# Optimization experiments

Hardware: AMD Instinct MI355X
Metric: run time of the kernel (lower is better)

Reference implementation:

```python
import jax, jax.numpy as jnp
import numpy as np

HIDDEN = 1024
HEADS = 16
HEAD_DIM = HIDDEN // HEADS


def setup_inputs() -> dict:
    key = jax.random.key(0)
    k0, k1, k2, k3, k4 = jax.random.split(key, 5)
    s = 0.02
    return {
        "data": jax.random.normal(k0, (4, 2048, HIDDEN), dtype=jnp.float32),
        "qkv_w": jax.random.normal(k1, (3 * HIDDEN, HIDDEN), dtype=jnp.float32) * s,  # (out,in) torch layout
        "qkv_b": jax.random.normal(k2, (3 * HIDDEN,), dtype=jnp.float32) * s,
        "out_w": jax.random.normal(k3, (HIDDEN, HIDDEN), dtype=jnp.float32) * s,
        "out_b": jax.random.normal(k4, (HIDDEN,), dtype=jnp.float32) * s,
    }


def reference(data, qkv_w, qkv_b, out_w, out_b):
    B, T, C = data.shape
    qkv = jnp.einsum("btc,oc->bto", data, qkv_w) + qkv_b  # [B,T,3C]
    q, k, v = jnp.split(qkv, 3, axis=2)
    # [B,T,C] -> [B,H,T,D]
    def heads(x):
        return x.reshape(B, T, HEADS, HEAD_DIM).transpose(0, 2, 1, 3)
    q, k, v = heads(q), heads(k), heads(v)
    scale = 1.0 / jnp.sqrt(jnp.float32(HEAD_DIM))
    att = jnp.einsum("bhqd,bhkd->bhqk", q, k) * scale  # [B,H,T,T]
    causal = jnp.tril(jnp.ones((T, T), dtype=bool))
    att = jnp.where(causal[None, None, :, :], att, -jnp.inf)
    att = jax.nn.softmax(att, axis=-1)
    out = jnp.einsum("bhqk,bhkd->bhqd", att, v)  # [B,H,T,D]
    out = out.transpose(0, 2, 1, 3).reshape(B, T, C)
    return jnp.einsum("btc,oc->bto", out, out_w) + out_b
```

## Files before the change

### kernel.cpp

```cpp
#include <hip/hip_runtime.h>
#include <hip/hip_bf16.h>
#include <stdint.h>

typedef __attribute__((ext_vector_type(8))) __bf16 bf16x8;
typedef __attribute__((ext_vector_type(4))) float f32x4;
typedef __attribute__((ext_vector_type(16))) float f32x16;
typedef __attribute__((ext_vector_type(4))) unsigned int u32x4;

#define HIDDEN 1024
#define HEADS 16
#define HD 64
#define NB 4
#define T_ 2048
#define M_ROWS (NB * T_)
#define SCL2 0.18033688f
#define FIXM 32.0f

__device__ __forceinline__ unsigned short f2bf(float x) {
  unsigned u = __builtin_bit_cast(unsigned, x);
  u += 0x7fff + ((u >> 16) & 1);
  return (unsigned short)(u >> 16);
}

__device__ __forceinline__ unsigned pk2(float a, float b) {
  unsigned ua = __builtin_bit_cast(unsigned, a) + 0x8000u;
  unsigned ub = __builtin_bit_cast(unsigned, b) + 0x8000u;
  return __builtin_amdgcn_perm(ub, ua, 0x07060302);
}

__device__ __forceinline__ f32x4 mfma16(bf16x8 a, bf16x8 b, f32x4 c) {
  return __builtin_amdgcn_mfma_f32_16x16x32_bf16(a, b, c, 0, 0, 0);
}
__device__ __forceinline__ f32x16 mfma32(bf16x8 a, bf16x8 b, f32x16 c) {
  return __builtin_amdgcn_mfma_f32_32x32x16_bf16(a, b, c, 0, 0, 0);
}

__device__ __forceinline__ void lds16(const void* g, void* l) {
  __builtin_amdgcn_global_load_lds(
      (const __attribute__((address_space(1))) unsigned int*)g,
      (__attribute__((address_space(3))) unsigned int*)l, 16, 0, 0);
}

__device__ __forceinline__ bf16x8 ldg8(const unsigned short* p) {
  return __builtin_bit_cast(bf16x8, *(const u32x4*)p);
}

__global__ void cvt_bf16(const float* __restrict__ in,
                         unsigned short* __restrict__ out, int n4) {
  int i = blockIdx.x * blockDim.x + threadIdx.x;
  int stride = gridDim.x * blockDim.x;
  for (; i < n4; i += stride) {
    float4 v = ((const float4*)in)[i];
    ushort4 o;
    o.x = f2bf(v.x); o.y = f2bf(v.y); o.z = f2bf(v.z); o.w = f2bf(v.w);
    ((ushort4*)out)[i] = o;
  }
}

template <int EPI>
__global__ __launch_bounds__(256) void gemm_bt(
    const unsigned short* __restrict__ A, const unsigned short* __restrict__ Bm,
    const float* __restrict__ bias, unsigned short* __restrict__ Qb,
    unsigned short* __restrict__ Kb, unsigned short* __restrict__ Vtb,
    float* __restrict__ Cf, int M, int N, int K) {
  __shared__ __align__(16) unsigned short Al[128 * 32];
  __shared__ __align__(16) unsigned short Bl[128 * 32];
  const int tid = threadIdx.x;
  const int w = tid >> 6, lane = tid & 63;
  const int l16 = lane & 15, grp = lane >> 4;
  const int brow0 = blockIdx.y * 128;
  const int bcol0 = blockIdx.x * 128;
  const int wrow = (w >> 1) * 64, wcol = (w & 1) * 64;

  f32x4 acc[4][4];
#pragma unroll
  for (int i = 0; i < 4; i++)
#pragma unroll
    for (int j = 0; j < 4; j++) acc[i][j] = (f32x4){0.f, 0.f, 0.f, 0.f};

  for (int k0 = 0; k0 < K; k0 += 32) {
    __syncthreads();
#pragma unroll
    for (int i = 0; i < 2; i++) {
      int off = (w * 2 + i) * 1024 + lane * 16;
      int row = off >> 6;
      int cole = (off & 63) >> 1;
      lds16(A + (size_t)(brow0 + row) * K + k0 + cole,
            (char*)Al + (w * 2 + i) * 1024);
      lds16(Bm + (size_t)(bcol0 + row) * K + k0 + cole,
            (char*)Bl + (w * 2 + i) * 1024);
    }
    __syncthreads();
    bf16x8 av[4], bv[4];
#pragma unroll
    for (int m = 0; m < 4; m++)
      av[m] = __builtin_bit_cast(
          bf16x8, *(const u32x4*)&Al[(wrow + m * 16 + l16) * 32 + grp * 8]);
#pragma unroll
    for (int n = 0; n < 4; n++)
      bv[n] = __builtin_bit_cast(
          bf16x8, *(const u32x4*)&Bl[(wcol + n * 16 + l16) * 32 + grp * 8]);
#pragma unroll
    for (int m = 0; m < 4; m++)
#pragma unroll
      for (int n = 0; n < 4; n++) acc[m][n] = mfma16(av[m], bv[n], acc[m][n]);
  }

#pragma unroll
  for (int m = 0; m < 4; m++) {
#pragma unroll
    for (int n = 0; n < 4; n++) {
      int col = bcol0 + wcol + n * 16 + l16;
      int row0 = brow0 + wrow + m * 16 + grp * 4;
      float bs = bias[col];
      if (EPI == 0) {
        int part = col >> 10, rem = col & 1023;
        int h = rem >> 6, d = rem & 63;
#pragma unroll
        for (int r = 0; r < 4; r++) {
          int rw = row0 + r;
          int b = rw >> 11, t = rw & 2047;
          unsigned short val = f2bf(acc[m][n][r] + bs);
          size_t bh = (size_t)(b * 16 + h);
          if (part == 0)
            Qb[(bh * T_ + t) * HD + d] = val;
          else if (part == 1)
            Kb[(bh * T_ + t) * HD + d] = val;
          else {
            int k = t & 31;
            int rr = (k & 3) + 4 * (k >> 3);
            int s = (rr & 7) + 8 * ((k >> 2) & 1) + 16 * (rr >> 3);
            Vtb[(bh * HD + d) * T_ + (t & ~31) + s] = val;
          }
        }
      } else {
#pragma unroll
        for (int r = 0; r < 4; r++)
          Cf[(size_t)(row0 + r) * N + col] = acc[m][n][r] + bs;
      }
    }
  }
}


__global__ __launch_bounds__(256, 3) void attn32(
    const unsigned short* __restrict__ Q, const unsigned short* __restrict__ K,
    const unsigned short* __restrict__ Vt, unsigned short* __restrict__ Ao) {
  __shared__ __align__(16) unsigned short Kl[2][32 * 64];
  __shared__ __align__(16) unsigned short Vl[2][32 * 64];
  const int i = blockIdx.x;
  const int bh = i & 63;
  const int g = (i < 512) ? (15 - (i >> 6)) : ((i - 512) >> 6);
  const int wv = threadIdx.x >> 6, lane = threadIdx.x & 63;
  const int l31 = lane & 31, hi = lane >> 5;
  const int qt = g * 4 + wv;
  const int maxqt = g * 4 + 3;
  const unsigned short* Qh = Q + (size_t)bh * T_ * HD;
  const unsigned short* Kh = K + (size_t)bh * T_ * HD;
  const unsigned short* Vh = Vt + (size_t)bh * HD * T_;
  const int b_ = bh >> 4, h_ = bh & 15;

  const int sj = threadIdx.x >> 3, su = threadIdx.x & 7;
  const int sup = su ^ (sj & 7);
  const unsigned short* ksrc = Kh + sj * HD + sup * 8;
  const unsigned short* vsrc =
      Vh + (size_t)(sj + 32 * (sup >> 2)) * T_ + (sup & 3) * 8;
  char* kdst0 = (char*)&Kl[0][0] + wv * 1024;
  char* kdst1 = (char*)&Kl[1][0] + wv * 1024;
  char* vdst0 = (char*)&Vl[0][0] + wv * 1024;
  char* vdst1 = (char*)&Vl[1][0] + wv * 1024;

#define STAGE(B, KC)                                         \
  do {                                                       \
    int kt_ = (KC) * 32;                                     \
    lds16(ksrc + (size_t)kt_ * HD, (B) ? kdst1 : kdst0);     \
    lds16(vsrc + kt_, (B) ? vdst1 : vdst0);                  \
  } while (0)

  int rdoff[4];
#pragma unroll
  for (int ks = 0; ks < 4; ks++)
    rdoff[ks] = l31 * 128 + (((2 * ks + hi) ^ (l31 & 7)) << 4);

  bf16x8 qf[4];
  const int qbase = qt * 32;
#pragma unroll
  for (int st = 0; st < 4; st++)
    qf[st] = ldg8(&Qh[(size_t)(qbase + l31) * HD + st * 16 + hi * 8]);

  f32x16 o0, o1;
#pragma unroll
  for (int r = 0; r < 16; r++) { o0[r] = 0.f; o1[r] = 0.f; }
  float rl = 0.f;

#define CHUNK(B, MASKED)                                                     \
  do {                                                                       \
    const char* kb = (const char*)&Kl[(B)][0];                               \
    const char* vb = (const char*)&Vl[(B)][0];                               \
    bf16x8 KF[4], VF[4];                                                     \
    _Pragma("unroll") for (int ks = 0; ks < 4; ks++) {                       \
      KF[ks] = __builtin_bit_cast(bf16x8, *(const u32x4*)(kb + rdoff[ks]));  \
      VF[ks] = __builtin_bit_cast(bf16x8, *(const u32x4*)(vb + rdoff[ks]));  \
    }                                                                        \
    f32x16 sa;                                                               \
    _Pragma("unroll") for (int r = 0; r < 16; r++) sa[r] = 0.f;              \
    sa = mfma32(KF[0], qf[0], sa);                                           \
    sa = mfma32(KF[1], qf[1], sa);                                           \
    sa = mfma32(KF[2], qf[2], sa);                                           \
    sa = mfma32(KF[3], qf[3], sa);                                           \
    float pv[16];                                                            \
    _Pragma("unroll") for (int r = 0; r < 16; r++) {                         \
      float arg = __builtin_fmaf(sa[r], SCL2, -FIXM);                        \
      if (MASKED) {                                                          \
        int key = (r & 3) + 8 * (r >> 2) + 4 * hi;                           \
        if (key > l31) arg = -1e30f;                                         \
      }                                                                      \
      pv[r] = exp2f(arg);                                                    \
      rl += pv[r];                                                           \
    }                                                                        \
    u32x4 pa0u, pa1u;                                                        \
    pa0u.x = pk2(pv[0], pv[1]);                                              \
    pa0u.y = pk2(pv[2], pv[3]);                                              \
    pa0u.z = pk2(pv[4], pv[5]);                                              \
    pa0u.w = pk2(pv[6], pv[7]);                                              \
    pa1u.x = pk2(pv[8], pv[9]);                                              \
    pa1u.y = pk2(pv[10], pv[11]);                                            \
    pa1u.z = pk2(pv[12], pv[13]);                                            \
    pa1u.w = pk2(pv[14], pv[15]);                                            \
    bf16x8 pa0 = __builtin_bit_cast(bf16x8, pa0u);                           \
    bf16x8 pa1 = __builtin_bit_cast(bf16x8, pa1u);                           \
    o0 = mfma32(VF[0], pa0, o0);                                             \
    o0 = mfma32(VF[1], pa1, o0);                                             \
    o1 = mfma32(VF[2], pa0, o1);                                             \
    o1 = mfma32(VF[3], pa1, o1);                                             \
  } while (0)

  STAGE(0, 0);
  __syncthreads();
  int cur = 0;
  for (int kc = 0; kc <= maxqt; kc++) {
    if (kc < maxqt) STAGE(cur ^ 1, kc + 1);
    if (kc < qt) {
      CHUNK(cur, 0);
    } else if (kc == qt) {
      CHUNK(cur, 1);
    }
    __syncthreads();
    cur ^= 1;
  }

  float rlt = rl + __shfl_xor(rl, 32);
  float inv = 1.f / rlt;
  const size_t base =
      ((size_t)b_ * T_ + qbase + l31) * HIDDEN + h_ * HD + hi * 4;
#pragma unroll
  for (int gg = 0; gg < 4; gg++) {
    uint2 u;
    u.x = pk2(o0[4 * gg] * inv, o0[4 * gg + 1] * inv);
    u.y = pk2(o0[4 * gg + 2] * inv, o0[4 * gg + 3] * inv);
    *(uint2*)&Ao[base + gg * 8] = u;
  }
#pragma unroll
  for (int gg = 0; gg < 4; gg++) {
    uint2 u;
    u.x = pk2(o1[4 * gg] * inv, o1[4 * gg + 1] * inv);
    u.y = pk2(o1[4 * gg + 2] * inv, o1[4 * gg + 3] * inv);
    *(uint2*)&Ao[base + 32 + gg * 8] = u;
  }
#undef STAGE
#undef CHUNK
}

extern "C" void kernel_launch(void* const* d_in, const int* in_sizes, int n_in,
                              void* d_out, int out_size, void* d_ws,
                              size_t ws_size, hipStream_t stream) {
  const float* data = (const float*)d_in[0];
  const float* qkvw = (const float*)d_in[1];
  const float* qkvb = (const float*)d_in[2];
  const float* outw = (const float*)d_in[3];
  const float* outb = (const float*)d_in[4];
  float* out = (float*)d_out;
  char* ws = (char*)d_ws;

  unsigned short* dataBf = (unsigned short*)(ws);
  unsigned short* qkvwBf = (unsigned short*)(ws + 16777216);
  unsigned short* outwBf = (unsigned short*)(ws + 23068672);
  unsigned short* Qb = (unsigned short*)(ws + 25165824);
  unsigned short* Kb = (unsigned short*)(ws + 41943040);
  unsigned short* Vtb = (unsigned short*)(ws + 58720256);
  unsigned short* attnO = dataBf;

  cvt_bf16<<<2048, 256, 0, stream>>>(data, dataBf, (M_ROWS * HIDDEN) / 4);
  cvt_bf16<<<1024, 256, 0, stream>>>(qkvw, qkvwBf, (3 * HIDDEN * HIDDEN) / 4);
  cvt_bf16<<<512, 256, 0, stream>>>(outw, outwBf, (HIDDEN * HIDDEN) / 4);

  gemm_bt<0><<<dim3(24, 64), 256, 0, stream>>>(dataBf, qkvwBf, qkvb, Qb, Kb,
                                               Vtb, nullptr, M_ROWS, 3 * HIDDEN,
                                               HIDDEN);
  attn32<<<1024, 256, 0, stream>>>(Qb, Kb, Vtb, attnO);
  gemm_bt<1><<<dim3(8, 64), 256, 0, stream>>>(attnO, outwBf, outb, nullptr,
                                              nullptr, nullptr, out, M_ROWS,
                                              HIDDEN, HIDDEN);
}
```

Baseline: 202.7 us.

## Replace GEMM with 256x128-tile, 8-wave, triple-buffered pipelined kernel

Replaces the simple 128x128 GEMM, which has two syncthreads per k-step, with a 512-thread kernel using 256x128 tiles and a K-step of 64. The k-loop is triple-buffered in shared memory with async global-to-LDS loads, XOR-swizzled LDS layout, and interleaved MFMA and LDS reads under s_setprio and barriers. It also remaps block ids for L2 locality. This aims to hide global load latency and raise MFMA utilization, at the cost of 144KB LDS per block, lower occupancy and hardcoded K/N sizes.

```diff
diff --git a/kernel.cpp b/kernel.cpp
--- a/kernel.cpp
+++ b/kernel.cpp
@@ -57,61 +57,156 @@
   }
 }
 
-template <int EPI>
-__global__ __launch_bounds__(256) void gemm_bt(
+
+#define MF4(AM, B0, B1, B2, B3, M)              \
+  acc[M][0] = mfma16(AM, B0, acc[M][0]);        \
+  acc[M][1] = mfma16(AM, B1, acc[M][1]);        \
+  acc[M][2] = mfma16(AM, B2, acc[M][2]);        \
+  acc[M][3] = mfma16(AM, B3, acc[M][3]);
+
+#define RD(BUF, OFF) \
+  __builtin_bit_cast(bf16x8, *(const u32x4*)((BUF) + (OFF)))
+
+template <int EPI, int NT>
+__global__ __launch_bounds__(512, 2) void gemm8(
     const unsigned short* __restrict__ A, const unsigned short* __restrict__ Bm,
     const float* __restrict__ bias, unsigned short* __restrict__ Qb,
     unsigned short* __restrict__ Kb, unsigned short* __restrict__ Vtb,
-    float* __restrict__ Cf, int M, int N, int K) {
-  __shared__ __align__(16) unsigned short Al[128 * 32];
-  __shared__ __align__(16) unsigned short Bl[128 * 32];
+    float* __restrict__ Cf) {
+  constexpr int K = 1024;
+  constexpr int N = NT * 128;
+  __shared__ __align__(16) char LB[147456];
   const int tid = threadIdx.x;
-  const int w = tid >> 6, lane = tid & 63;
+  const int wv = tid >> 6, lane = tid & 63;
   const int l16 = lane & 15, grp = lane >> 4;
-  const int brow0 = blockIdx.y * 128;
-  const int bcol0 = blockIdx.x * 128;
-  const int wrow = (w >> 1) * 64, wcol = (w & 1) * 64;
+  const int wm = wv >> 1, wn = wv & 1;
+  const int bid = blockIdx.x;
+  const int sw = (bid & 7) * (NT * 4) + (bid >> 3);
+  const int by = sw / NT, bx = sw % NT;
+  const int brow0 = by * 256, bcol0 = bx * 128;
+
+  const int srow = wv * 8 + (lane >> 3);
+  const int sunit = (lane & 7) ^ (srow & 7);
+  const unsigned short* pA = A + (size_t)(brow0 + srow) * K + sunit * 8;
+  const unsigned short* pB = Bm + (size_t)(bcol0 + srow) * K + sunit * 8;
+
+  const int rsw = l16 & 7;
+  const int swu0 = ((grp) ^ rsw) << 4;
+  const int swu1 = ((4 + grp) ^ rsw) << 4;
+  const int aBase = (wm * 64 + l16) * 128;
+  const int bBase = (wn * 64 + l16) * 128;
+
+#define BUFA(c) (LB + (c) * 49152)
+#define BUFB(c) (LB + (c) * 49152 + 32768)
+#define STAGE_A01(c, t)                                          \
+  do {                                                           \
+    lds16(pA + (size_t)(t) * 64, BUFA(c) + wv * 1024);           \
+    lds16(pA + (size_t)64 * K + (t) * 64,                        \
+          BUFA(c) + 8192 + wv * 1024);                           \
+  } while (0)
+#define STAGE_A23(c, t)                                          \
+  do {                                                           \
+    lds16(pA + (size_t)128 * K + (t) * 64,                       \
+          BUFA(c) + 16384 + wv * 1024);                          \
+    lds16(pA + (size_t)192 * K + (t) * 64,                       \
+          BUFA(c) + 24576 + wv * 1024);                          \
+  } while (0)
+#define STAGE_B01(c, t)                                          \
+  do {                                                           \
+    lds16(pB + (size_t)(t) * 64, BUFB(c) + wv * 1024);           \
+    lds16(pB + (size_t)64 * K + (t) * 64,                        \
+          BUFB(c) + 8192 + wv * 1024);                           \
+  } while (0)
 
   f32x4 acc[4][4];
 #pragma unroll
-  for (int i = 0; i < 4; i++)
-#pragma unroll
-    for (int j = 0; j < 4; j++) acc[i][j] = (f32x4){0.f, 0.f, 0.f, 0.f};
-
-  for (int k0 = 0; k0 < K; k0 += 32) {
-    __syncthreads();
-#pragma unroll
-    for (int i = 0; i < 2; i++) {
-      int off = (w * 2 + i) * 1024 + lane * 16;
-      int row = off >> 6;
-      int cole = (off & 63) >> 1;
-      lds16(A + (size_t)(brow0 + row) * K + k0 + cole,
-            (char*)Al + (w * 2 + i) * 1024);
-      lds16(Bm + (size_t)(bcol0 + row) * K + k0 + cole,
-            (char*)Bl + (w * 2 + i) * 1024);
-    }
-    __syncthreads();
-    bf16x8 av[4], bv[4];
-#pragma unroll
-    for (int m = 0; m < 4; m++)
-      av[m] = __builtin_bit_cast(
-          bf16x8, *(const u32x4*)&Al[(wrow + m * 16 + l16) * 32 + grp * 8]);
-#pragma unroll
-    for (int n = 0; n < 4; n++)
-      bv[n] = __builtin_bit_cast(
-          bf16x8, *(const u32x4*)&Bl[(wcol + n * 16 + l16) * 32 + grp * 8]);
-#pragma unroll
-    for (int m = 0; m < 4; m++)
-#pragma unroll
-      for (int n = 0; n < 4; n++) acc[m][n] = mfma16(av[m], bv[n], acc[m][n]);
+  for (int m = 0; m < 4; m++)
+#pragma unroll
+    for (int n = 0; n < 4; n++) acc[m][n] = (f32x4){0.f, 0.f, 0.f, 0.f};
+
+#define GTILE(BA, BB, S1, S2, S3, ENDW)                                \
+  {                                                                    \
+    bf16x8 b00 = RD(BB, bBase + swu0), b01 = RD(BB, bBase + 2048 + swu0), \
+           b02 = RD(BB, bBase + 4096 + swu0),                          \
+           b03 = RD(BB, bBase + 6144 + swu0);                          \
+    bf16x8 a0 = RD(BA, aBase + swu0), a1 = RD(BA, aBase + 2048 + swu0); \
+    S1;                                                                \
+    __builtin_amdgcn_s_barrier();                                      \
+    __builtin_amdgcn_s_setprio(1);                                     \
+    MF4(a0, b00, b01, b02, b03, 0)                                     \
+    MF4(a1, b00, b01, b02, b03, 1)                                     \
+    __builtin_amdgcn_s_setprio(0);                                     \
+    __builtin_amdgcn_s_barrier();                                      \
+    bf16x8 b10 = RD(BB, bBase + swu1), b11 = RD(BB, bBase + 2048 + swu1), \
+           b12 = RD(BB, bBase + 4096 + swu1),                          \
+           b13 = RD(BB, bBase + 6144 + swu1);                          \
+    a0 = RD(BA, aBase + swu1);                                         \
+    a1 = RD(BA, aBase + 2048 + swu1);                                  \
+    S2;                                                                \
+    __builtin_amdgcn_s_barrier();                                      \
+    __builtin_amdgcn_s_setprio(1);                                     \
+    MF4(a0, b10, b11, b12, b13, 0)                                     \
+    MF4(a1, b10, b11, b12, b13, 1)                                     \
+    __builtin_amdgcn_s_setprio(0);                                     \
+    __builtin_amdgcn_s_barrier();                                      \
+    a0 = RD(BA, aBase + 4096 + swu0);                                  \
+    a1 = RD(BA, aBase + 6144 + swu0);                                  \
+    S3;                                                                \
+    __builtin_amdgcn_s_barrier();                                      \
+    __builtin_amdgcn_s_setprio(1);                                     \
+    MF4(a0, b00, b01, b02, b03, 2)                                     \
+    MF4(a1, b00, b01, b02, b03, 3)                                     \
+    __builtin_amdgcn_s_setprio(0);                                     \
+    __builtin_amdgcn_s_barrier();                                      \
+    a0 = RD(BA, aBase + 4096 + swu1);                                  \
+    a1 = RD(BA, aBase + 6144 + swu1);                                  \
+    __builtin_amdgcn_s_barrier();                                      \
+    __builtin_amdgcn_s_setprio(1);                                     \
+    MF4(a0, b10, b11, b12, b13, 2)                                     \
+    MF4(a1, b10, b11, b12, b13, 3)                                     \
+    __builtin_amdgcn_s_setprio(0);                                     \
+    ENDW;                                                              \
+    __builtin_amdgcn_s_barrier();                                      \
+  }
+
+  STAGE_A01(0, 0); STAGE_A23(0, 0); STAGE_B01(0, 0);
+  STAGE_A01(1, 1); STAGE_A23(1, 1); STAGE_B01(1, 1);
+  asm volatile("s_waitcnt vmcnt(6)" ::: "memory");
+  __builtin_amdgcn_sched_barrier(0);
+  __builtin_amdgcn_s_barrier();
+
+  int c = 0, c2 = 2;
+#pragma unroll 1
+  for (int t = 0; t < 14; ++t) {
+    const char* ba = BUFA(c);
+    const char* bb = BUFB(c);
+    GTILE(ba, bb, STAGE_A01(c2, t + 2), STAGE_A23(c2, t + 2),
+          STAGE_B01(c2, t + 2),
+          { asm volatile("s_waitcnt vmcnt(6)" ::: "memory");
+            __builtin_amdgcn_sched_barrier(0); });
+    c = (c == 2) ? 0 : c + 1;
+    c2 = (c2 == 2) ? 0 : c2 + 1;
+  }
+  {
+    const char* ba = BUFA(c);
+    const char* bb = BUFB(c);
+    GTILE(ba, bb, , , ,
+          { asm volatile("s_waitcnt vmcnt(0)" ::: "memory");
+            __builtin_amdgcn_sched_barrier(0); });
+    c = (c == 2) ? 0 : c + 1;
+  }
+  {
+    const char* ba = BUFA(c);
+    const char* bb = BUFB(c);
+    GTILE(ba, bb, , , , );
   }
 
 #pragma unroll
   for (int m = 0; m < 4; m++) {
 #pragma unroll
     for (int n = 0; n < 4; n++) {
-      int col = bcol0 + wcol + n * 16 + l16;
-      int row0 = brow0 + wrow + m * 16 + grp * 4;
+      int col = bcol0 + wn * 64 + n * 16 + l16;
+      int row0 = brow0 + wm * 64 + m * 16 + grp * 4;
       float bs = bias[col];
       if (EPI == 0) {
         int part = col >> 10, rem = col & 1023;
@@ -140,8 +235,13 @@
       }
     }
   }
-}
-
+#undef BUFA
+#undef BUFB
+#undef STAGE_A01
+#undef STAGE_A23
+#undef STAGE_B01
+#undef GTILE
+}
 
 __global__ __launch_bounds__(256, 3) void attn32(
     const unsigned short* __restrict__ Q, const unsigned short* __restrict__ K,
@@ -170,11 +270,11 @@
   char* vdst0 = (char*)&Vl[0][0] + wv * 1024;
   char* vdst1 = (char*)&Vl[1][0] + wv * 1024;
 
-#define STAGE(B, KC)                                         \
-  do {                                                       \
-    int kt_ = (KC) * 32;                                     \
-    lds16(ksrc + (size_t)kt_ * HD, (B) ? kdst1 : kdst0);     \
-    lds16(vsrc + kt_, (B) ? vdst1 : vdst0);                  \
+#define STAGE(B, KC)                                     \
+  do {                                                   \
+    int kt_ = (KC) * 32;                                 \
+    lds16(ksrc + (size_t)kt_ * HD, (B) ? kdst1 : kdst0); \
+    lds16(vsrc + kt_, (B) ? vdst1 : vdst0);              \
   } while (0)
 
   int rdoff[4];
@@ -294,11 +394,9 @@
   cvt_bf16<<<1024, 256, 0, stream>>>(qkvw, qkvwBf, (3 * HIDDEN * HIDDEN) / 4);
   cvt_bf16<<<512, 256, 0, stream>>>(outw, outwBf, (HIDDEN * HIDDEN) / 4);
 
-  gemm_bt<0><<<dim3(24, 64), 256, 0, stream>>>(dataBf, qkvwBf, qkvb, Qb, Kb,
-                                               Vtb, nullptr, M_ROWS, 3 * HIDDEN,
-                                               HIDDEN);
+  gemm8<0, 24><<<768, 512, 0, stream>>>(dataBf, qkvwBf, qkvb, Qb, Kb, Vtb,
+                                        nullptr);
   attn32<<<1024, 256, 0, stream>>>(Qb, Kb, Vtb, attnO);
-  gemm_bt<1><<<dim3(8, 64), 256, 0, stream>>>(attnO, outwBf, outb, nullptr,
-                                              nullptr, nullptr, out, M_ROWS,
-                                              HIDDEN, HIDDEN);
-}
+  gemm8<1, 8><<<256, 512, 0, stream>>>(attnO, outwBf, outb, nullptr, nullptr,
+                                       nullptr, out);
+}
```

Measured after the change: 188.1 us. 7.2% less time.

## Rewrite projection GEMMs with 3-stage LDS pipeline, 128x256 tiles and swizzling

Applied to the files above, without the earlier changes.

Replaces the simple double-sync GEMM with an 8-wave 128x256 tile kernel that prefetches two k-steps ahead through a three-buffer LDS ring, using manual waitcnt and barriers. It also swizzles LDS layout to avoid bank conflicts, remaps block IDs for L2 locality, and raises MFMA priority. The aim is to hide global load latency behind MFMA work and cut per-iteration synchronisation. In exchange it uses more LDS per block, and it hardcodes K=1024 plus the grid sizes.

```diff
diff --git a/kernel.cpp b/kernel.cpp
--- a/kernel.cpp
+++ b/kernel.cpp
@@ -57,61 +57,93 @@
   }
 }
 
-template <int EPI>
-__global__ __launch_bounds__(256) void gemm_bt(
+
+#define RD(BUF, OFF) \
+  __builtin_bit_cast(bf16x8, *(const u32x4*)((BUF) + (OFF)))
+
+template <int EPI, int NT>
+__global__ __launch_bounds__(512, 4) void gemm8(
     const unsigned short* __restrict__ A, const unsigned short* __restrict__ Bm,
     const float* __restrict__ bias, unsigned short* __restrict__ Qb,
     unsigned short* __restrict__ Kb, unsigned short* __restrict__ Vtb,
-    float* __restrict__ Cf, int M, int N, int K) {
-  __shared__ __align__(16) unsigned short Al[128 * 32];
-  __shared__ __align__(16) unsigned short Bl[128 * 32];
+    float* __restrict__ Cf) {
+  constexpr int K = 1024;
+  constexpr int N = NT * 256;
+  __shared__ __align__(16) char LB[3][24576];
   const int tid = threadIdx.x;
-  const int w = tid >> 6, lane = tid & 63;
+  const int wv = tid >> 6, lane = tid & 63;
   const int l16 = lane & 15, grp = lane >> 4;
-  const int brow0 = blockIdx.y * 128;
-  const int bcol0 = blockIdx.x * 128;
-  const int wrow = (w >> 1) * 64, wcol = (w & 1) * 64;
+  const int wm = wv >> 2, wn = wv & 3;
+  const int bid = blockIdx.x;
+  const int sw = (bid & 7) * ((64 * NT) >> 3) + (bid >> 3);
+  const int by = sw / NT, bx = sw % NT;
+  const int brow0 = by * 128, bcol0 = bx * 256;
+
+  const int ua = (tid & 7) ^ ((tid >> 3) & 7);
+  const unsigned short* aptr =
+      A + (size_t)(brow0 + (tid >> 3) * 2 + (ua >> 2)) * K + (ua & 3) * 8;
+  const unsigned short* bptr =
+      Bm + (size_t)(bcol0 + (tid >> 3) * 2 + (ua >> 2)) * K + (ua & 3) * 8;
+
+  const int swu = ((((l16 & 1) * 4) + grp) ^ ((l16 >> 1) & 7)) * 16;
+  const int aoff = (wm * 32 + (l16 >> 1)) * 128 + swu;
+  const int boff = 8192 + (wn * 32 + (l16 >> 1)) * 128 + swu;
+
+#define STAGE(c, t)                                                   \
+  do {                                                                \
+    lds16(aptr + (size_t)(t) * 32, (char*)LB[c] + wv * 1024);         \
+    lds16(bptr + (size_t)(t) * 32, (char*)LB[c] + 8192 + wv * 1024);  \
+    lds16(bptr + (size_t)128 * K + (size_t)(t) * 32,                  \
+          (char*)LB[c] + 16384 + wv * 1024);                          \
+  } while (0)
 
   f32x4 acc[4][4];
 #pragma unroll
-  for (int i = 0; i < 4; i++)
-#pragma unroll
-    for (int j = 0; j < 4; j++) acc[i][j] = (f32x4){0.f, 0.f, 0.f, 0.f};
-
-  for (int k0 = 0; k0 < K; k0 += 32) {
-    __syncthreads();
-#pragma unroll
-    for (int i = 0; i < 2; i++) {
-      int off = (w * 2 + i) * 1024 + lane * 16;
-      int row = off >> 6;
-      int cole = (off & 63) >> 1;
-      lds16(A + (size_t)(brow0 + row) * K + k0 + cole,
-            (char*)Al + (w * 2 + i) * 1024);
-      lds16(Bm + (size_t)(bcol0 + row) * K + k0 + cole,
-            (char*)Bl + (w * 2 + i) * 1024);
+  for (int m = 0; m < 4; m++)
+#pragma unroll
+    for (int n = 0; n < 4; n++) acc[m][n] = (f32x4){0.f, 0.f, 0.f, 0.f};
+
+  STAGE(0, 0);
+  STAGE(1, 1);
+  asm volatile("s_waitcnt vmcnt(3)" ::: "memory");
+  __builtin_amdgcn_sched_barrier(0);
+  __builtin_amdgcn_s_barrier();
+
+  int c = 0, c2 = 2;
+#pragma unroll 1
+  for (int t = 0; t < 32; ++t) {
+    const char* buf = (const char*)LB[c];
+    bf16x8 bf[4], af[4];
+#pragma unroll
+    for (int n = 0; n < 4; n++) bf[n] = RD(buf, boff + n * 1024);
+#pragma unroll
+    for (int m = 0; m < 4; m++) af[m] = RD(buf, aoff + m * 1024);
+    if (t < 30) STAGE(c2, t + 2);
+    __builtin_amdgcn_s_barrier();
+    __builtin_amdgcn_s_setprio(1);
+#pragma unroll
+    for (int m = 0; m < 4; m++)
+#pragma unroll
+      for (int n = 0; n < 4; n++) acc[m][n] = mfma16(af[m], bf[n], acc[m][n]);
+    __builtin_amdgcn_s_setprio(0);
+    if (t < 30) {
+      asm volatile("s_waitcnt vmcnt(3)" ::: "memory");
+      __builtin_amdgcn_sched_barrier(0);
+    } else if (t == 30) {
+      asm volatile("s_waitcnt vmcnt(0)" ::: "memory");
+      __builtin_amdgcn_sched_barrier(0);
     }
-    __syncthreads();
-    bf16x8 av[4], bv[4];
-#pragma unroll
-    for (int m = 0; m < 4; m++)
-      av[m] = __builtin_bit_cast(
-          bf16x8, *(const u32x4*)&Al[(wrow + m * 16 + l16) * 32 + grp * 8]);
-#pragma unroll
-    for (int n = 0; n < 4; n++)
-      bv[n] = __builtin_bit_cast(
-          bf16x8, *(const u32x4*)&Bl[(wcol + n * 16 + l16) * 32 + grp * 8]);
-#pragma unroll
-    for (int m = 0; m < 4; m++)
-#pragma unroll
-      for (int n = 0; n < 4; n++) acc[m][n] = mfma16(av[m], bv[n], acc[m][n]);
+    if (t < 31) __builtin_amdgcn_s_barrier();
+    c = (c == 2) ? 0 : c + 1;
+    c2 = (c2 == 2) ? 0 : c2 + 1;
   }
 
 #pragma unroll
   for (int m = 0; m < 4; m++) {
 #pragma unroll
     for (int n = 0; n < 4; n++) {
-      int col = bcol0 + wcol + n * 16 + l16;
-      int row0 = brow0 + wrow + m * 16 + grp * 4;
+      int col = bcol0 + wn * 64 + n * 16 + l16;
+      int row0 = brow0 + wm * 64 + m * 16 + grp * 4;
       float bs = bias[col];
       if (EPI == 0) {
         int part = col >> 10, rem = col & 1023;
@@ -140,8 +172,8 @@
       }
     }
   }
-}
-
+#undef STAGE
+}
 
 __global__ __launch_bounds__(256, 3) void attn32(
     const unsigned short* __restrict__ Q, const unsigned short* __restrict__ K,
@@ -170,11 +202,11 @@
   char* vdst0 = (char*)&Vl[0][0] + wv * 1024;
   char* vdst1 = (char*)&Vl[1][0] + wv * 1024;
 
-#define STAGE(B, KC)                                         \
-  do {                                                       \
-    int kt_ = (KC) * 32;                                     \
-    lds16(ksrc + (size_t)kt_ * HD, (B) ? kdst1 : kdst0);     \
-    lds16(vsrc + kt_, (B) ? vdst1 : vdst0);                  \
+#define STAGE(B, KC)                                     \
+  do {                                                   \
+    int kt_ = (KC) * 32;                                 \
+    lds16(ksrc + (size_t)kt_ * HD, (B) ? kdst1 : kdst0); \
+    lds16(vsrc + kt_, (B) ? vdst1 : vdst0);              \
   } while (0)
 
   int rdoff[4];
@@ -294,11 +326,9 @@
   cvt_bf16<<<1024, 256, 0, stream>>>(qkvw, qkvwBf, (3 * HIDDEN * HIDDEN) / 4);
   cvt_bf16<<<512, 256, 0, stream>>>(outw, outwBf, (HIDDEN * HIDDEN) / 4);
 
-  gemm_bt<0><<<dim3(24, 64), 256, 0, stream>>>(dataBf, qkvwBf, qkvb, Qb, Kb,
-                                               Vtb, nullptr, M_ROWS, 3 * HIDDEN,
-                                               HIDDEN);
+  gemm8<0, 12><<<768, 512, 0, stream>>>(dataBf, qkvwBf, qkvb, Qb, Kb, Vtb,
+                                        nullptr);
   attn32<<<1024, 256, 0, stream>>>(Qb, Kb, Vtb, attnO);
-  gemm_bt<1><<<dim3(8, 64), 256, 0, stream>>>(attnO, outwBf, outb, nullptr,
-                                              nullptr, nullptr, out, M_ROWS,
-                                              HIDDEN, HIDDEN);
-}
+  gemm8<1, 4><<<256, 512, 0, stream>>>(attnO, outwBf, outb, nullptr, nullptr,
+                                       nullptr, out);
+}
```

New measurement: 198.3 us. 1.02x faster.
